# Optimization experiments

Measured on AMD Instinct MI355X. Metric: run time of the kernel, lower is better.

The kernel has to match this reference:

```python
import jax, jax.numpy as jnp
import numpy as np

B = 32
N_PER = 4096
N = B * N_PER
E = 2_097_152
D_IN = 32
D_OUT = 32
NUM_G_RELS = 14
NUM_ATTN_RELS = 10


def setup_inputs() -> dict:
    key = jax.random.key(0)
    ks = jax.random.split(key, 12)
    feat = jax.random.normal(ks[0], (N, D_IN), jnp.float32)
    src = jax.random.randint(ks[1], (E,), 0, N)
    dst = jax.random.randint(ks[2], (E,), 0, N)
    etype = jax.random.randint(ks[3], (E,), 0, NUM_ATTN_RELS)
    norm = jax.random.uniform(ks[4], (E,), jnp.float32)
    index1 = jax.random.randint(ks[5], (N,), 0, 2)  # path-node mask
    # first NUM_G_RELS nodes of each subgraph carry distinct relation slots -> unique scatter indices
    index2 = jnp.tile((jnp.arange(N_PER) < NUM_G_RELS).astype(jnp.int32), B)
    f2 = jnp.tile(jnp.arange(N_PER) % NUM_G_RELS, B).astype(jnp.int32)
    tar_rel = jnp.tile((jnp.arange(N_PER) == 0).astype(jnp.int32), B)  # one target node per graph
    s = 0.1
    W_w = jax.random.normal(ks[6], (D_IN, D_OUT), jnp.float32) * s
    b_w = jnp.zeros((D_OUT,), jnp.float32)
    W2 = jax.random.normal(ks[7], (3 * D_OUT, D_OUT), jnp.float32) * s
    b2 = jnp.zeros((D_OUT,), jnp.float32)
    attn_rel_emb = jax.random.normal(ks[8], (NUM_ATTN_RELS, D_OUT), jnp.float32) * s
    self_loop_w = jax.random.normal(ks[9], (D_IN, D_OUT), jnp.float32) * s
    W_line = jax.random.normal(ks[10], (D_OUT, D_OUT), jnp.float32) * s
    b_line = jnp.zeros((D_OUT,), jnp.float32)
    zero_path = jax.random.normal(ks[11], (1, D_OUT), jnp.float32) * s
    return {"feat": feat, "norm": norm, "W_w": W_w, "b_w": b_w, "W2": W2, "b2": b2,
            "attn_rel_emb": attn_rel_emb, "self_loop_w": self_loop_w, "W_line": W_line,
            "b_line": b_line, "zero_path": zero_path, "src": src, "dst": dst, "etype": etype,
            "index1": index1, "index2": index2, "f2": f2, "tar_rel": tar_rel,
            "n_per": N_PER, "num_g_rels": NUM_G_RELS}


def reference(feat, norm, W_w, b_w, W2, b2, attn_rel_emb, self_loop_w, W_line, b_line,
              zero_path, src, dst, etype, index1, index2, f2, tar_rel, n_per, num_g_rels):
    n_nodes, _ = feat.shape
    D = W_w.shape[1]
    # --- edge-wise relation-gated MLP (msg_func) ---
    et = attn_rel_emb[etype]                       # [E, D]
    w1 = feat[src] @ W_w + b_w                     # [E, D]
    cat = jnp.concatenate([et + w1, et - w1, et * w1], axis=1)  # [E, 3D]
    msg = (cat @ W2 + b2) * norm[:, None]          # [E, D] (edge weight w == 1)
    # --- SumAggregator: sum of msgs (alpha = ones) + self-loop term ---
    h = jax.ops.segment_sum(msg, dst, num_segments=n_nodes) + feat @ self_loop_w
    nf = jax.nn.relu(h @ W_line + b_line)          # cg_node_feats [N, D]
    # --- per-subgraph relation scatter + path attention (vectorized over batch) ---
    Bn = n_nodes // n_per
    nf_b = nf.reshape(Bn, n_per, D)
    mask2 = index2.reshape(Bn, n_per) != 0
    f2b = f2.reshape(Bn, n_per) + 1                # index_offset = 1
    write_idx = jnp.where(mask2, f2b, num_g_rels + 1)  # route masked rows to dump slot

    def scatter_one(idx, feats):
        buf = jnp.zeros((num_g_rels + 2, D), nf.dtype).at[idx].set(feats)
        return buf[:num_g_rels + 1]

    batch_rel_emds = jax.vmap(scatter_one)(write_idx, nf_b)  # [B, num_g_rels+1, D]
    tar1 = (tar_rel.reshape(Bn, n_per) == 1).astype(nf.dtype)
    target_rel_emd = jnp.einsum('bn,bnd->bd', tar1, nf_b)    # [B, D] (one-hot select)
    p1 = index1.reshape(Bn, n_per) == 1
    scores = jnp.where(p1, jnp.einsum('bnd,bd->bn', nf_b, target_rel_emd), -1e30)
    alpha = jax.nn.softmax(scores, axis=1)                   # segmented softmax over path nodes
    agg = jnp.einsum('bn,bnd->bd', alpha, nf_b)
    path_agg_emd = jnp.where(p1.any(axis=1)[:, None], agg, zero_path)  # [B, D]
    return batch_rel_emds, target_rel_emd, path_agg_emd
```

## Files before the change

### kernel.cpp

```cpp
#include <hip/hip_runtime.h>


#define N_PER_C 4096
#define NGR 14
#define NAR 10
#define NZB 68
#define KSP 8
#define BKN 128
#define NBMAX 1024
#define TSC 4096
#define CHK 2560

typedef unsigned short u16;
typedef unsigned int u32;
typedef _Float16 hv2 __attribute__((ext_vector_type(2)));
union U32H2 { u32 u; hv2 h; };

__device__ __forceinline__ float b2f(u16 u) {
    union { u32 i; float f; } x; x.i = ((u32)u) << 16; return x.f;
}
__device__ __forceinline__ u16 f2bf(float f) {
    union { float f; u32 i; } x; x.f = f;
    u32 r = x.i + 0x7fff + ((x.i >> 16) & 1);
    return (u16)(r >> 16);
}
__device__ __forceinline__ float LD(const void* p, size_t i, int isf32) {
    return isf32 ? ((const float*)p)[i] : b2f(((const u16*)p)[i]);
}
__device__ __forceinline__ void ST_OUT(void* p, size_t i, float v, int isf32) {
    if (isf32) ((float*)p)[i] = v;
    else ((u16*)p)[i] = f2bf(v);
}
__device__ __forceinline__ u32 pkh(float a, float b) {
    U32H2 c; c.h = (hv2){(_Float16)a, (_Float16)b}; return c.u;
}
__device__ __forceinline__ hv2 ash2(u32 w) { U32H2 c; c.u = w; return c.h; }

__device__ __forceinline__ int probe_flag(const u32* featw) {
    int cnt = 0;
#pragma unroll
    for (int i = 0; i < 256; i += 64) {
        u32 w = featw[i + (threadIdx.x & 63)];
        u32 lo = w & 0xffffu;
        u32 e = (lo >> 7) & 0xffu;
        cnt += ((e >= 100 && e <= 140) || lo == 0) ? 1 : 0;
    }
    unsigned long long m = __ballot(cnt >= 3);
    return (__popcll(m) < 32) ? 1 : 0;
}

__global__ __launch_bounds__(256) void k_prep(
        const u32* __restrict__ featw,
        const void* W_w, const void* b_w, const void* W2, const void* b2v,
        const void* attn, const void* slw, const void* W_line, const void* b_line,
        u32* __restrict__ outw, int out_size,
        float* Wwf, float* bwf, float* Af, float* slwf, float* Wlf, float* blf,
        float* Cf, float* ctf, u32* at2, u32* bcur, int NB,
        int* done, int Bn, int* flag) {
    int t = threadIdx.x;
    int b = blockIdx.x;
    int isf32 = probe_flag(featw);
    if (b < NZB) {
        int words = isf32 ? out_size : out_size / 2;
        for (int i = b * 256 + t; i < words; i += NZB * 256) outw[i] = 0;
        for (int i = b * 256 + t; i < NB; i += NZB * 256) bcur[i] = 0u;
        for (int i = b * 256 + t; i < Bn; i += NZB * 256) done[i] = 0;
        return;
    }
    if (t == 0) flag[0] = isf32;
    for (int i = t; i < 1024; i += 256) {
        int k = i >> 5, c = i & 31;
        Wwf[i]  = LD(W_w, i, isf32);
        slwf[i] = LD(slw, i, isf32);
        Wlf[i]  = LD(W_line, i, isf32);
        Af[i]   = LD(W2, k * 32 + c, isf32) - LD(W2, (32 + k) * 32 + c, isf32);
        Cf[i]   = LD(W2, (64 + k) * 32 + c, isf32);
    }
    for (int i = t; i < NAR * 16; i += 256) {
        int tt = i >> 4, q = i & 15;
        at2[i] = pkh(LD(attn, tt * 32 + 2 * q, isf32),
                     LD(attn, tt * 32 + 2 * q + 1, isf32));
    }
    for (int i = t; i < NAR * 32; i += 256) {
        int tt = i >> 5, j = i & 31;
        float s = LD(b2v, j, isf32);
        for (int k = 0; k < 32; ++k) {
            float a = LD(attn, tt * 32 + k, isf32);
            s += a * (LD(W2, k * 32 + j, isf32) + LD(W2, (32 + k) * 32 + j, isf32));
        }
        ctf[i] = s;
    }
    if (t < 32) { bwf[t] = LD(b_w, t, isf32); blf[t] = LD(b_line, t, isf32); }
}

__global__ __launch_bounds__(256) void k1_node(const void* __restrict__ feat,
                        const float* __restrict__ Wwf,
                        const float* __restrict__ bwf, const float* __restrict__ slwf,
                        u32* __restrict__ gbuf, u32* __restrict__ h, int N,
                        const int* __restrict__ flag) {
    int gid = blockIdx.x * 256 + threadIdx.x;
    if (gid >= N) return;
    int isf32 = flag[0];
    int n = gid;
    float f[32];
    if (isf32) {
        const float4* fr = (const float4*)((const float*)feat + (size_t)n * 32);
#pragma unroll
        for (int q = 0; q < 8; ++q) {
            float4 v = fr[q];
            f[q * 4 + 0] = v.x; f[q * 4 + 1] = v.y; f[q * 4 + 2] = v.z; f[q * 4 + 3] = v.w;
        }
    } else {
        const uint4* fr = (const uint4*)((const u16*)feat + (size_t)n * 32);
#pragma unroll
        for (int q = 0; q < 4; ++q) {
            uint4 v = fr[q];
            u32 ww[4] = {v.x, v.y, v.z, v.w};
#pragma unroll
            for (int r = 0; r < 4; ++r) {
                f[q * 8 + 2 * r]     = b2f((u16)(ww[r] & 0xffff));
                f[q * 8 + 2 * r + 1] = b2f((u16)(ww[r] >> 16));
            }
        }
    }
    float g[32], hh[32];
#pragma unroll
    for (int j = 0; j < 32; ++j) { g[j] = bwf[j]; hh[j] = 0.f; }
#pragma unroll
    for (int k = 0; k < 32; ++k) {
        float fk = f[k];
#pragma unroll
        for (int j = 0; j < 32; ++j) {
            g[j]  += fk * Wwf[k * 32 + j];
            hh[j] += fk * slwf[k * 32 + j];
        }
    }
    u32* go = gbuf + (size_t)n * 16;
#pragma unroll
    for (int q = 0; q < 16; ++q) go[q] = pkh(g[2 * q], g[2 * q + 1]);
    u32* ho = h + (size_t)n * 16;
#pragma unroll
    for (int q = 0; q < 16; ++q) ho[q] = pkh(hh[2 * q], hh[2 * q + 1]);
}

__global__ __launch_bounds__(256) void kB_scatter(const int* __restrict__ src,
        const int* __restrict__ dst, const int* __restrict__ et,
        const void* __restrict__ norm, u32* __restrict__ bcur,
        uint2* __restrict__ pay, int E, int NB, int CAP,
        const int* __restrict__ flag) {
    __shared__ u32 lcnt[NBMAX], loffA[NBMAX], loffB[NBMAX], lbase[NBMAX];
    __shared__ u32 red[256];
    __shared__ uint2 lbuf[TSC];
    __shared__ u16 lbkt[TSC];
    int tid = threadIdx.x;
    int base_e = blockIdx.x * TSC;
    int nval = E - base_e; if (nval > TSC) nval = TSC; if (nval < 0) nval = 0;
    int isf32 = flag[0];
    for (int i = tid; i < NB; i += 256) lcnt[i] = 0u;
    __syncthreads();
    u32 pk0[16], nw[16]; int bk[16];
#pragma unroll
    for (int i = 0; i < 16; ++i) {
        int e = base_e + i * 256 + tid;
        if (e < E) {
            int s = src[e], d = dst[e], t = et[e];
            float nr = LD(norm, e, isf32);
            pk0[i] = (u32)s | ((u32)t << 17) | ((u32)(d & (BKN - 1)) << 21);
            nw[i] = __float_as_uint(nr);
            bk[i] = ((u32)d) / BKN;
            atomicAdd(&lcnt[bk[i]], 1u);
        } else bk[i] = -1;
    }
    __syncthreads();
    u32 c4[4]; u32 s = 0;
#pragma unroll
    for (int k = 0; k < 4; ++k) {
        int idx = tid * 4 + k;
        c4[k] = (idx < NB) ? lcnt[idx] : 0u;
        s += c4[k];
    }
    red[tid] = s;
    __syncthreads();
    for (int off = 1; off < 256; off <<= 1) {
        u32 v = (tid >= off) ? red[tid - off] : 0u;
        __syncthreads();
        red[tid] += v;
        __syncthreads();
    }
    u32 ex = red[tid] - s;
#pragma unroll
    for (int k = 0; k < 4; ++k) {
        int idx = tid * 4 + k;
        if (idx < NB) { loffA[idx] = ex; loffB[idx] = ex; ex += c4[k]; }
    }
    __syncthreads();
    for (int b = tid; b < NB; b += 256) {
        u32 c = lcnt[b];
        if (c) lbase[b] = atomicAdd(&bcur[b], c);
    }
    __syncthreads();
#pragma unroll
    for (int i = 0; i < 16; ++i) {
        if (bk[i] >= 0) {
            u32 slot = atomicAdd(&loffB[bk[i]], 1u);
            lbuf[slot] = make_uint2(pk0[i], nw[i]);
            lbkt[slot] = (u16)bk[i];
        }
    }
    __syncthreads();
    for (int s2 = tid; s2 < nval; s2 += 256) {
        int b = lbkt[s2];
        u32 loc = lbase[b] + (u32)s2 - loffA[b];
        if (loc < (u32)CAP) pay[(size_t)b * CAP + loc] = lbuf[s2];
    }
}

__global__ __launch_bounds__(128) void kC_bucket(const u32* __restrict__ gbuf,
        const uint2* __restrict__ pay, const u32* __restrict__ bcur,
        const float* __restrict__ Af, const float* __restrict__ Cf,
        const float* __restrict__ ctf, const u32* __restrict__ at2,
        u32* __restrict__ h, int CAP) {
    __shared__ uint2 lbuf[CHK];
    __shared__ u32 cnt_s[BKN];
    __shared__ u32 off_s[BKN];
    __shared__ u32 cur_s[BKN];
    __shared__ u32 scn_s[BKN];
    __shared__ u32 atl[16 * NAR];
    int tid = threadIdx.x;
    int b = blockIdx.x;
    for (int i = tid; i < 16 * NAR; i += 128) {
        int t = i >> 4, q = i & 15;
        atl[q * NAR + t] = at2[i];
    }
    int e0 = b * CAP;
    u32 tot = bcur[b]; if (tot > (u32)CAP) tot = (u32)CAP;
    int e1 = e0 + (int)tot;

    float yg[32], x[32], nt[NAR];
#pragma unroll
    for (int j = 0; j < 32; ++j) { yg[j] = 0.f; x[j] = 0.f; }
#pragma unroll
    for (int t = 0; t < NAR; ++t) nt[t] = 0.f;

    for (int cb = e0; cb < e1; cb += CHK) {
        int nrec = e1 - cb; if (nrec > CHK) nrec = CHK;
        cnt_s[tid] = 0u;
        __syncthreads();
        for (int i = tid; i < nrec; i += 128)
            atomicAdd(&cnt_s[(pay[cb + i].x >> 21) & (BKN - 1)], 1u);
        __syncthreads();
        u32 myv = cnt_s[tid];
        scn_s[tid] = myv;
        __syncthreads();
        for (int s = 1; s < BKN; s <<= 1) {
            u32 v = (tid >= s) ? scn_s[tid - s] : 0u;
            __syncthreads();
            scn_s[tid] += v;
            __syncthreads();
        }
        u32 myoff = scn_s[tid] - myv;
        off_s[tid] = myoff;
        cur_s[tid] = myoff;
        __syncthreads();
        for (int i = tid; i < nrec; i += 128) {
            uint2 r = pay[cb + i];
            u32 d = (r.x >> 21) & (BKN - 1);
            u32 slot = atomicAdd(&cur_s[d], 1u);
            lbuf[slot] = r;
        }
        __syncthreads();
        {
            u32 myc = myv;
            uint2 rec = make_uint2(0u, 0u);
            uint4 GA = {0,0,0,0}, GB = {0,0,0,0}, GC = {0,0,0,0}, GD = {0,0,0,0};
            if (myc) {
                rec = lbuf[myoff];
                const uint4* g4 = (const uint4*)(gbuf + (size_t)(rec.x & 0x1FFFFu) * 16);
                GA = g4[0]; GB = g4[1]; GC = g4[2]; GD = g4[3];
            }
            for (u32 r = 0; r < myc; ++r) {
                uint2 rn = make_uint2(0u, 0u);
                uint4 HA = {0,0,0,0}, HB = {0,0,0,0}, HC = {0,0,0,0}, HD = {0,0,0,0};
                if (r + 1 < myc) {
                    rn = lbuf[myoff + r + 1];
                    const uint4* g4 = (const uint4*)(gbuf + (size_t)(rn.x & 0x1FFFFu) * 16);
                    HA = g4[0]; HB = g4[1]; HC = g4[2]; HD = g4[3];
                }
                int t = (int)((rec.x >> 17) & 0xFu);
                float nr = __uint_as_float(rec.y);
                u32 gw[16] = {GA.x, GA.y, GA.z, GA.w, GB.x, GB.y, GB.z, GB.w,
                              GC.x, GC.y, GC.z, GC.w, GD.x, GD.y, GD.z, GD.w};
#pragma unroll
                for (int q = 0; q < 16; ++q) {
                    hv2 gv = ash2(gw[q]);
                    hv2 av = ash2(atl[q * NAR + t]);
                    float ng0 = nr * (float)gv[0];
                    float ng1 = nr * (float)gv[1];
                    yg[2 * q]     += ng0;
                    yg[2 * q + 1] += ng1;
                    x[2 * q]      += ng0 * (float)av[0];
                    x[2 * q + 1]  += ng1 * (float)av[1];
                }
#pragma unroll
                for (int t2 = 0; t2 < NAR; ++t2) nt[t2] += (t2 == t) ? nr : 0.f;
                rec = rn;
                GA = HA; GB = HB; GC = HC; GD = HD;
            }
        }
        __syncthreads();
    }

    int n = b * BKN + tid;
    float o[32];
    const uint4* hr4 = (const uint4*)(h + (size_t)n * 16);
    uint4 v0 = hr4[0], v1 = hr4[1], v2 = hr4[2], v3 = hr4[3];
    u32 ww[16] = {v0.x, v0.y, v0.z, v0.w, v1.x, v1.y, v1.z, v1.w,
                  v2.x, v2.y, v2.z, v2.w, v3.x, v3.y, v3.z, v3.w};
#pragma unroll
    for (int r = 0; r < 16; ++r) {
        hv2 xh = ash2(ww[r]);
        o[2 * r]     = (float)xh[0];
        o[2 * r + 1] = (float)xh[1];
    }
#pragma unroll
    for (int t = 0; t < NAR; ++t) {
        float w = nt[t];
#pragma unroll
        for (int j = 0; j < 32; ++j) o[j] += w * ctf[t * 32 + j];
    }
#pragma unroll
    for (int k = 0; k < 32; ++k) {
        float a = yg[k], c = x[k];
#pragma unroll
        for (int j = 0; j < 32; ++j)
            o[j] += a * Af[k * 32 + j] + c * Cf[k * 32 + j];
    }
    u32* ho = h + (size_t)n * 16;
#pragma unroll
    for (int q = 0; q < 16; ++q) ho[q] = pkh(o[2 * q], o[2 * q + 1]);
}

__global__ __launch_bounds__(256) void k34_fused(const u32* __restrict__ h,
        const float* __restrict__ Wlf, const float* __restrict__ blf,
        const int* __restrict__ index2, const int* __restrict__ f2,
        const int* __restrict__ index1, const void* __restrict__ zero_path,
        void* __restrict__ out, size_t off_tar, size_t off_path,
        float* __restrict__ part_m, float* __restrict__ part_l,
        float* __restrict__ part_a, int* __restrict__ done,
        const int* __restrict__ flag) {
    int blk = blockIdx.x;
    int b = blk / KSP, c = blk % KSP;
    int tid = threadIdx.x;
    int isf32 = flag[0];
    __shared__ float tg[32];
    __shared__ float red_m[256], red_l[256];
    __shared__ float red_a[256][33];
    __shared__ int last_s;

    if (tid < 32) {
        const u32* h0 = h + (size_t)b * N_PER_C * 16;
        float o = blf[tid];
#pragma unroll
        for (int k = 0; k < 32; ++k) {
            hv2 x = ash2(h0[k >> 1]);
            o += (float)x[k & 1] * Wlf[k * 32 + tid];
        }
        o = fmaxf(o, 0.f);
        tg[tid] = o;
        if (c == 0) ST_OUT(out, off_tar + (size_t)b * 32 + tid, o, isf32);
    }
    __syncthreads();
    float tv[32];
#pragma unroll
    for (int j = 0; j < 32; ++j) tv[j] = tg[j];

    float m = -1e30f, l = 0.f, a[32];
#pragma unroll
    for (int j = 0; j < 32; ++j) a[j] = 0.f;

    const int R = N_PER_C / KSP;
    for (int rr = 0; rr < R / 256; ++rr) {
        int n = b * N_PER_C + c * R + rr * 256 + tid;
        float hr[32];
        const uint4* h4 = (const uint4*)(h + (size_t)n * 16);
#pragma unroll
        for (int q = 0; q < 4; ++q) {
            uint4 v = h4[q];
            u32 ww[4] = {v.x, v.y, v.z, v.w};
#pragma unroll
            for (int r2 = 0; r2 < 4; ++r2) {
                hv2 x = ash2(ww[r2]);
                hr[q * 8 + 2 * r2]     = (float)x[0];
                hr[q * 8 + 2 * r2 + 1] = (float)x[1];
            }
        }
        float o[32];
#pragma unroll
        for (int j = 0; j < 32; ++j) o[j] = blf[j];
#pragma unroll
        for (int k = 0; k < 32; ++k) {
            float hk = hr[k];
#pragma unroll
            for (int j = 0; j < 32; ++j) o[j] += hk * Wlf[k * 32 + j];
        }
#pragma unroll
        for (int j = 0; j < 32; ++j) o[j] = fmaxf(o[j], 0.f);
        if (index2[n] != 0) {
            int idx = f2[n] + 1;
            if (idx >= 0 && idx <= NGR) {
                size_t bse = ((size_t)(b * (NGR + 1) + idx)) * 32;
#pragma unroll
                for (int j = 0; j < 32; ++j) ST_OUT(out, bse + j, o[j], isf32);
            }
        }
        if (index1[n] == 1) {
            float dot = 0.f;
#pragma unroll
            for (int j = 0; j < 32; ++j) dot += o[j] * tv[j];
            if (dot > m) {
                float cc = __expf(m - dot);
                l *= cc;
#pragma unroll
                for (int j = 0; j < 32; ++j) a[j] *= cc;
                m = dot;
            }
            float w = __expf(dot - m);
            l += w;
#pragma unroll
            for (int j = 0; j < 32; ++j) a[j] += w * o[j];
        }
    }
    red_m[tid] = m; red_l[tid] = l;
#pragma unroll
    for (int j = 0; j < 32; ++j) red_a[tid][j] = a[j];
    __syncthreads();
    for (int s = 128; s >= 1; s >>= 1) {
        if (tid < s) {
            float m1 = red_m[tid], m2 = red_m[tid + s];
            float M = fmaxf(m1, m2);
            float c1 = __expf(m1 - M), c2 = __expf(m2 - M);
            red_l[tid] = red_l[tid] * c1 + red_l[tid + s] * c2;
#pragma unroll
            for (int j = 0; j < 32; ++j)
                red_a[tid][j] = red_a[tid][j] * c1 + red_a[tid + s][j] * c2;
            red_m[tid] = M;
        }
        __syncthreads();
    }
    if (tid == 0) { part_m[blk] = red_m[0]; part_l[blk] = red_l[0]; }
    if (tid < 32) part_a[(size_t)blk * 32 + tid] = red_a[0][tid];
    __syncthreads();
    if (tid == 0) {
        __threadfence();
        last_s = (atomicAdd(&done[b], 1) == KSP - 1);
    }
    __syncthreads();
    if (last_s) {
        __threadfence();
        if (tid < 32) {
            int j = tid;
            float M = -1e30f;
#pragma unroll
            for (int i = 0; i < KSP; ++i) M = fmaxf(M, part_m[b * KSP + i]);
            float L = 0.f, A = 0.f;
#pragma unroll
            for (int i = 0; i < KSP; ++i) {
                float cc = __expf(part_m[b * KSP + i] - M);
                L += part_l[b * KSP + i] * cc;
                A += part_a[(size_t)(b * KSP + i) * 32 + j] * cc;
            }
            float o = (L > 0.f) ? (A / L) : LD(zero_path, j, isf32);
            ST_OUT(out, off_path + (size_t)b * 32 + j, o, isf32);
        }
    }
}

extern "C" void kernel_launch(void* const* d_in, const int* in_sizes, int n_in,
                              void* d_out, int out_size, void* d_ws, size_t ws_size,
                              hipStream_t stream) {
    const void* feat     = d_in[0];
    const void* norm     = d_in[1];
    const void* W_w      = d_in[2];
    const void* b_w      = d_in[3];
    const void* W2       = d_in[4];
    const void* b2v      = d_in[5];
    const void* attn     = d_in[6];
    const void* slw      = d_in[7];
    const void* W_line   = d_in[8];
    const void* b_line   = d_in[9];
    const void* zeroPath = d_in[10];
    const int* src       = (const int*)d_in[11];
    const int* dst       = (const int*)d_in[12];
    const int* etype     = (const int*)d_in[13];
    const int* index1    = (const int*)d_in[14];
    const int* index2    = (const int*)d_in[15];
    const int* f2        = (const int*)d_in[16];

    int N  = in_sizes[0] / 32;
    int E  = in_sizes[1];
    int Bn = N / N_PER_C;
    int NB = N / BKN;
    int CAP = (((E / NB) * 5) / 4 + 255) & ~255;
    if (CAP > CHK) CAP = CHK;

    char* base  = (char*)d_ws;
    int* flag   = (int*)base;
    float* Wwf  = (float*)(base + 64);
    float* bwf  = Wwf + 1024;
    float* Af   = bwf + 32;
    float* slwf = Af + 1024;
    float* Wlf  = slwf + 1024;
    float* blf  = Wlf + 1024;
    float* Cf   = blf + 32;
    float* ctf  = Cf + 1024;
    u32*  at2   = (u32*)(ctf + NAR * 32);
    float* part_m = (float*)(at2 + NAR * 16);
    float* part_l = part_m + (size_t)Bn * KSP;
    float* part_a = part_l + (size_t)Bn * KSP;
    int* done   = (int*)(part_a + (size_t)Bn * KSP * 32);
    char* pa = (char*)(done + Bn);
    pa = (char*)(((size_t)pa + 255) & ~(size_t)255);
    u32* bcur  = (u32*)pa;
    char* pb = (char*)(bcur + NBMAX);
    pb = (char*)(((size_t)pb + 255) & ~(size_t)255);
    uint2* pay  = (uint2*)pb;
    u32* gbuf   = (u32*)(pay + (size_t)NB * CAP);
    u32* h      = gbuf + (size_t)N * 16;

    size_t off_tar  = (size_t)Bn * (NGR + 1) * 32;
    size_t off_path = off_tar + (size_t)Bn * 32;

    k_prep<<<NZB + 1, 256, 0, stream>>>((const u32*)feat,
                                        W_w, b_w, W2, b2v, attn, slw, W_line, b_line,
                                        (u32*)d_out, out_size,
                                        Wwf, bwf, Af, slwf, Wlf, blf,
                                        Cf, ctf, at2, bcur, NB, done, Bn, flag);
    k1_node<<<(N + 255) / 256, 256, 0, stream>>>(feat, Wwf, bwf, slwf, gbuf, h, N,
                                                 flag);
    kB_scatter<<<(E + TSC - 1) / TSC, 256, 0, stream>>>(src, dst, etype, norm,
                                                        bcur, pay, E, NB, CAP,
                                                        flag);
    kC_bucket<<<NB, 128, 0, stream>>>(gbuf, pay, bcur, Af, Cf, ctf, at2, h, CAP);
    k34_fused<<<Bn * KSP, 256, 0, stream>>>(h, Wlf, blf, index2, f2, index1,
                                            zeroPath, d_out, off_tar, off_path,
                                            part_m, part_l, part_a, done, flag);
}
```

Before: 267.8 us.

## Fuse node transform into edge scatter and use wave-shuffle softmax reduction

The per-node feature transform kernel is merged into the edge bucket-scatter kernel. The grid is the larger of the two original grids, and each block does its node rows before its edge tile. This removes one launch and lets the two independent phases share blocks. Separately, the path-attention kernel splits each subgraph into 16 chunks instead of 8, so each thread handles one row. Its 256-wide shared-memory tree reduction of the online-softmax state is replaced by a cross-lane shuffle reduction within each wavefront plus a small four-wave merge, which cuts LDS traffic and barriers. The cost is more partial results to merge in the last block, and the fused kernel's shared-memory footprint now applies to the node phase too.

```diff
diff --git a/kernel.cpp b/kernel.cpp
--- a/kernel.cpp
+++ b/kernel.cpp
@@ -5,7 +5,7 @@
 #define NGR 14
 #define NAR 10
 #define NZB 68
-#define KSP 8
+#define KSP 16
 #define BKN 128
 #define NBMAX 1024
 #define TSC 4096
@@ -93,69 +93,67 @@
     if (t < 32) { bwf[t] = LD(b_w, t, isf32); blf[t] = LD(b_line, t, isf32); }
 }
 
-__global__ __launch_bounds__(256) void k1_node(const void* __restrict__ feat,
-                        const float* __restrict__ Wwf,
-                        const float* __restrict__ bwf, const float* __restrict__ slwf,
-                        u32* __restrict__ gbuf, u32* __restrict__ h, int N,
-                        const int* __restrict__ flag) {
-    int gid = blockIdx.x * 256 + threadIdx.x;
-    if (gid >= N) return;
-    int isf32 = flag[0];
-    int n = gid;
-    float f[32];
-    if (isf32) {
-        const float4* fr = (const float4*)((const float*)feat + (size_t)n * 32);
-#pragma unroll
-        for (int q = 0; q < 8; ++q) {
-            float4 v = fr[q];
-            f[q * 4 + 0] = v.x; f[q * 4 + 1] = v.y; f[q * 4 + 2] = v.z; f[q * 4 + 3] = v.w;
-        }
-    } else {
-        const uint4* fr = (const uint4*)((const u16*)feat + (size_t)n * 32);
-#pragma unroll
-        for (int q = 0; q < 4; ++q) {
-            uint4 v = fr[q];
-            u32 ww[4] = {v.x, v.y, v.z, v.w};
-#pragma unroll
-            for (int r = 0; r < 4; ++r) {
-                f[q * 8 + 2 * r]     = b2f((u16)(ww[r] & 0xffff));
-                f[q * 8 + 2 * r + 1] = b2f((u16)(ww[r] >> 16));
-            }
-        }
-    }
-    float g[32], hh[32];
-#pragma unroll
-    for (int j = 0; j < 32; ++j) { g[j] = bwf[j]; hh[j] = 0.f; }
-#pragma unroll
-    for (int k = 0; k < 32; ++k) {
-        float fk = f[k];
-#pragma unroll
-        for (int j = 0; j < 32; ++j) {
-            g[j]  += fk * Wwf[k * 32 + j];
-            hh[j] += fk * slwf[k * 32 + j];
-        }
-    }
-    u32* go = gbuf + (size_t)n * 16;
-#pragma unroll
-    for (int q = 0; q < 16; ++q) go[q] = pkh(g[2 * q], g[2 * q + 1]);
-    u32* ho = h + (size_t)n * 16;
-#pragma unroll
-    for (int q = 0; q < 16; ++q) ho[q] = pkh(hh[2 * q], hh[2 * q + 1]);
-}
-
-__global__ __launch_bounds__(256) void kB_scatter(const int* __restrict__ src,
-        const int* __restrict__ dst, const int* __restrict__ et,
-        const void* __restrict__ norm, u32* __restrict__ bcur,
-        uint2* __restrict__ pay, int E, int NB, int CAP,
+__global__ __launch_bounds__(256) void k1b(const void* __restrict__ feat,
+        const float* __restrict__ Wwf, const float* __restrict__ bwf,
+        const float* __restrict__ slwf,
+        u32* __restrict__ gbuf, u32* __restrict__ h, int N,
+        const int* __restrict__ src, const int* __restrict__ dst,
+        const int* __restrict__ et, const void* __restrict__ norm,
+        u32* __restrict__ bcur, uint2* __restrict__ pay, int E, int NB, int CAP,
         const int* __restrict__ flag) {
     __shared__ u32 lcnt[NBMAX], loffA[NBMAX], loffB[NBMAX], lbase[NBMAX];
     __shared__ u32 red[256];
     __shared__ uint2 lbuf[TSC];
     __shared__ u16 lbkt[TSC];
     int tid = threadIdx.x;
+    int isf32 = flag[0];
+
+    int gid = blockIdx.x * 256 + tid;
+    if (gid < N) {
+        int n = gid;
+        float f[32];
+        if (isf32) {
+            const float4* fr = (const float4*)((const float*)feat + (size_t)n * 32);
+#pragma unroll
+            for (int q = 0; q < 8; ++q) {
+                float4 v = fr[q];
+                f[q * 4 + 0] = v.x; f[q * 4 + 1] = v.y; f[q * 4 + 2] = v.z; f[q * 4 + 3] = v.w;
+            }
+        } else {
+            const uint4* fr = (const uint4*)((const u16*)feat + (size_t)n * 32);
+#pragma unroll
+            for (int q = 0; q < 4; ++q) {
+                uint4 v = fr[q];
+                u32 ww[4] = {v.x, v.y, v.z, v.w};
+#pragma unroll
+                for (int r = 0; r < 4; ++r) {
+                    f[q * 8 + 2 * r]     = b2f((u16)(ww[r] & 0xffff));
+                    f[q * 8 + 2 * r + 1] = b2f((u16)(ww[r] >> 16));
+                }
+            }
+        }
+        float g[32], hh[32];
+#pragma unroll
+        for (int j = 0; j < 32; ++j) { g[j] = bwf[j]; hh[j] = 0.f; }
+#pragma unroll
+        for (int k = 0; k < 32; ++k) {
+            float fk = f[k];
+#pragma unroll
+            for (int j = 0; j < 32; ++j) {
+                g[j]  += fk * Wwf[k * 32 + j];
+                hh[j] += fk * slwf[k * 32 + j];
+            }
+        }
+        u32* go = gbuf + (size_t)n * 16;
+#pragma unroll
+        for (int q = 0; q < 16; ++q) go[q] = pkh(g[2 * q], g[2 * q + 1]);
+        u32* ho = h + (size_t)n * 16;
+#pragma unroll
+        for (int q = 0; q < 16; ++q) ho[q] = pkh(hh[2 * q], hh[2 * q + 1]);
+    }
+
     int base_e = blockIdx.x * TSC;
     int nval = E - base_e; if (nval > TSC) nval = TSC; if (nval < 0) nval = 0;
-    int isf32 = flag[0];
     for (int i = tid; i < NB; i += 256) lcnt[i] = 0u;
     __syncthreads();
     u32 pk0[16], nw[16]; int bk[16];
@@ -353,8 +351,7 @@
     int tid = threadIdx.x;
     int isf32 = flag[0];
     __shared__ float tg[32];
-    __shared__ float red_m[256], red_l[256];
-    __shared__ float red_a[256][33];
+    __shared__ float wm[4], wl[4], wa[4][32];
     __shared__ int last_s;
 
     if (tid < 32) {
@@ -379,8 +376,8 @@
     for (int j = 0; j < 32; ++j) a[j] = 0.f;
 
     const int R = N_PER_C / KSP;
-    for (int rr = 0; rr < R / 256; ++rr) {
-        int n = b * N_PER_C + c * R + rr * 256 + tid;
+    {
+        int n = b * N_PER_C + c * R + tid;
         float hr[32];
         const uint4* h4 = (const uint4*)(h + (size_t)n * 16);
 #pragma unroll
@@ -417,38 +414,45 @@
             float dot = 0.f;
 #pragma unroll
             for (int j = 0; j < 32; ++j) dot += o[j] * tv[j];
-            if (dot > m) {
-                float cc = __expf(m - dot);
-                l *= cc;
-#pragma unroll
-                for (int j = 0; j < 32; ++j) a[j] *= cc;
-                m = dot;
-            }
-            float w = __expf(dot - m);
-            l += w;
-#pragma unroll
-            for (int j = 0; j < 32; ++j) a[j] += w * o[j];
-        }
-    }
-    red_m[tid] = m; red_l[tid] = l;
-#pragma unroll
-    for (int j = 0; j < 32; ++j) red_a[tid][j] = a[j];
-    __syncthreads();
-    for (int s = 128; s >= 1; s >>= 1) {
-        if (tid < s) {
-            float m1 = red_m[tid], m2 = red_m[tid + s];
-            float M = fmaxf(m1, m2);
-            float c1 = __expf(m1 - M), c2 = __expf(m2 - M);
-            red_l[tid] = red_l[tid] * c1 + red_l[tid + s] * c2;
-#pragma unroll
-            for (int j = 0; j < 32; ++j)
-                red_a[tid][j] = red_a[tid][j] * c1 + red_a[tid + s][j] * c2;
-            red_m[tid] = M;
-        }
-        __syncthreads();
-    }
-    if (tid == 0) { part_m[blk] = red_m[0]; part_l[blk] = red_l[0]; }
-    if (tid < 32) part_a[(size_t)blk * 32 + tid] = red_a[0][tid];
+            m = dot;
+            l = 1.f;
+#pragma unroll
+            for (int j = 0; j < 32; ++j) a[j] = o[j];
+        }
+    }
+#pragma unroll
+    for (int s = 1; s < 64; s <<= 1) {
+        float m2 = __shfl_xor(m, s);
+        float l2 = __shfl_xor(l, s);
+        float M = fmaxf(m, m2);
+        float c1 = __expf(m - M), c2 = __expf(m2 - M);
+        l = l * c1 + l2 * c2;
+#pragma unroll
+        for (int j = 0; j < 32; ++j) {
+            float a2 = __shfl_xor(a[j], s);
+            a[j] = a[j] * c1 + a2 * c2;
+        }
+        m = M;
+    }
+    {
+        int w = tid >> 6, lane = tid & 63;
+        if (lane < 32) wa[w][lane] = a[lane];
+        if (lane == 0) { wm[w] = m; wl[w] = l; }
+    }
+    __syncthreads();
+    if (tid < 32) {
+        int j = tid;
+        float M = fmaxf(fmaxf(wm[0], wm[1]), fmaxf(wm[2], wm[3]));
+        float L = 0.f, A = 0.f;
+#pragma unroll
+        for (int i = 0; i < 4; ++i) {
+            float cc = __expf(wm[i] - M);
+            L += wl[i] * cc;
+            A += wa[i][j] * cc;
+        }
+        if (j == 0) { part_m[blk] = M; part_l[blk] = L; }
+        part_a[(size_t)blk * 32 + j] = A;
+    }
     __syncthreads();
     if (tid == 0) {
         __threadfence();
@@ -530,16 +534,18 @@
     size_t off_tar  = (size_t)Bn * (NGR + 1) * 32;
     size_t off_path = off_tar + (size_t)Bn * 32;
 
+    int gridAB = (N + 255) / 256;
+    int gridB  = (E + TSC - 1) / TSC;
+    if (gridB > gridAB) gridAB = gridB;
+
     k_prep<<<NZB + 1, 256, 0, stream>>>((const u32*)feat,
                                         W_w, b_w, W2, b2v, attn, slw, W_line, b_line,
                                         (u32*)d_out, out_size,
                                         Wwf, bwf, Af, slwf, Wlf, blf,
                                         Cf, ctf, at2, bcur, NB, done, Bn, flag);
-    k1_node<<<(N + 255) / 256, 256, 0, stream>>>(feat, Wwf, bwf, slwf, gbuf, h, N,
-                                                 flag);
-    kB_scatter<<<(E + TSC - 1) / TSC, 256, 0, stream>>>(src, dst, etype, norm,
-                                                        bcur, pay, E, NB, CAP,
-                                                        flag);
+    k1b<<<gridAB, 256, 0, stream>>>(feat, Wwf, bwf, slwf, gbuf, h, N,
+                                    src, dst, etype, norm, bcur, pay, E, NB, CAP,
+                                    flag);
     kC_bucket<<<NB, 128, 0, stream>>>(gbuf, pay, bcur, Af, Cf, ctf, at2, h, CAP);
     k34_fused<<<Bn * KSP, 256, 0, stream>>>(h, Wlf, blf, index2, f2, index1,
                                             zeroPath, d_out, off_tar, off_path,
```

New measurement: 257.8 us, median of 2. 3.7% less time.
